# Performance work log

Measured on AMD Instinct MI355X. Metric: run time of the kernel, lower is better.

Reference implementation:

```python
import jax, jax.numpy as jnp
import numpy as np
from jax import lax

E, H, D = 1024, 16, 64          # embed_dim, num_heads, head_dim
B, T = 8, 64                    # batch, decode chunk
KV = 4096                       # kv_seq_len -> cache capacity 2*KV
START = 4096                    # start_pos (prefill already filled cache[:START])
THETA = 10000.0


def setup_inputs() -> dict:
    key = jax.random.key(0)
    kx, kck, kcv, kq, kk, kv, ko = jax.random.split(key, 7)
    s = 0.02
    return {
        "x": jax.random.normal(kx, (B, T, E), jnp.float32),
        "cache_keys": jax.random.normal(kck, (B, 2 * KV, H, D), jnp.float32),
        "cache_values": jax.random.normal(kcv, (B, 2 * KV, H, D), jnp.float32),
        "Wq": jax.random.normal(kq, (E, E), jnp.float32) * s,
        "Wk": jax.random.normal(kk, (E, E), jnp.float32) * s,
        "Wv": jax.random.normal(kv, (E, E), jnp.float32) * s,
        "Wo": jax.random.normal(ko, (E, E), jnp.float32) * s,
        "start_pos": START,
    }


def _rope_bug_faithful(x, start_pos):
    # x: (B, T, H, Dd). The source helper unpacks (B,H,T,D)=x.shape on a (B,T,H,D)
    # tensor, so rotation angles are indexed by HEAD index (positions
    # start_pos..start_pos+H-1) and broadcast over the time axis. Reproduced exactly.
    Bn, Tn, Hn, Dd = x.shape
    dh = Dd // 2
    inv_freq = 1.0 / (THETA ** (jnp.arange(dh, dtype=jnp.float32) / dh))
    pos = jnp.arange(Hn, dtype=jnp.float32) + jnp.float32(start_pos)  # (H,)
    ang = pos[:, None] * inv_freq[None, :]                            # (H, dh)
    cos = jnp.cos(ang)[None, None]                                    # (1,1,H,dh)
    sin = jnp.sin(ang)[None, None]
    xr = x.reshape(Bn, Tn, Hn, dh, 2)
    x0, x1 = xr[..., 0], xr[..., 1]
    o0 = x0 * cos - x1 * sin
    o1 = x0 * sin + x1 * cos
    return jnp.stack([o0, o1], axis=-1).reshape(Bn, Tn, Hn, Dd)


def reference(x, cache_keys, cache_values, Wq, Wk, Wv, Wo, start_pos):
    Bn, Tn, C = x.shape
    Hn, Dd = cache_keys.shape[2], cache_keys.shape[3]
    scale = 1.0 / np.sqrt(Dd).astype(np.float32)
    end = start_pos + Tn

    q = (x @ Wq).reshape(Bn, Tn, Hn, Dd)
    k = (x @ Wk).reshape(Bn, Tn, Hn, Dd)
    v = (x @ Wv).reshape(Bn, Tn, Hn, Dd)

    q = _rope_bug_faithful(q, start_pos)
    k = _rope_bug_faithful(k, start_pos)

    # cache append at dynamic offset (detached in source)
    ck = lax.dynamic_update_slice_in_dim(cache_keys, lax.stop_gradient(k), start_pos, axis=1)
    cv = lax.dynamic_update_slice_in_dim(cache_values, lax.stop_gradient(v), start_pos, axis=1)
    k_full = lax.stop_gradient(ck[:, :end])  # (B, S, H, D), S = end
    v_full = lax.stop_gradient(cv[:, :end])

    qh = q.transpose(0, 2, 1, 3)        # (B,H,T,D)
    kh = k_full.transpose(0, 2, 1, 3)   # (B,H,S,D)
    vh = v_full.transpose(0, 2, 1, 3)

    scores = jnp.einsum("bhtd,bhsd->bhts", qh, kh) * scale  # (B,H,T,S)
    i = jnp.arange(Tn)[:, None]
    j = jnp.arange(end)[None, :]
    allowed = j <= (start_pos + i)      # intended causal mask over cache span
    neg = jnp.finfo(scores.dtype).min
    scores = jnp.where(allowed[None, None], scores, neg)
    attn = jax.nn.softmax(scores, axis=-1)
    ctx = jnp.einsum("bhts,bhsd->bhtd", attn, vh)
    out = ctx.transpose(0, 2, 1, 3).reshape(Bn, Tn, C) @ Wo
    return out
```

## Files before the change

kernel.cpp:

```cpp
#include <hip/hip_runtime.h>
#include <hip/hip_bf16.h>
#include <math.h>

typedef __attribute__((ext_vector_type(8))) __bf16 bf16x8;
typedef __attribute__((ext_vector_type(4))) __bf16 bf16x4;
typedef __attribute__((ext_vector_type(4))) float f32x4;

#define EE 1024
#define HH 16
#define DD 64
#define BB 8
#define TT 64
#define NSPLIT 8

__device__ __forceinline__ f32x4 mfma16(bf16x8 a, bf16x8 b, f32x4 c) {
    return __builtin_amdgcn_mfma_f32_16x16x32_bf16(a, b, c, 0, 0, 0);
}

__global__ __launch_bounds__(256) void k_prep(const float* __restrict__ Wq, const float* __restrict__ Wk,
                                              const float* __restrict__ Wv, const float* __restrict__ Wo,
                                              __bf16* __restrict__ WT) {
    __shared__ float tile[64][68];
    int bid = blockIdx.x;
    int w = bid >> 8, tl = bid & 255;
    int k0 = (tl >> 4) * 64, n0 = (tl & 15) * 64;
    const float* W = (w == 0) ? Wq : (w == 1) ? Wk : (w == 2) ? Wv : Wo;
    int tid = threadIdx.x;
#pragma unroll
    for (int p = 0; p < 4; ++p) {
        int idx = p * 256 + tid;
        int r = idx >> 4, c4 = (idx & 15) * 4;
        float4 f = *(const float4*)&W[(size_t)(k0 + r) * EE + n0 + c4];
        *(float4*)&tile[r][c4] = f;
    }
    __syncthreads();
    __bf16* out = WT + (size_t)w * EE * EE;
#pragma unroll
    for (int p = 0; p < 2; ++p) {
        int q = p * 256 + tid;
        int r = q >> 3, c8 = (q & 7) * 8;
        bf16x8 v;
#pragma unroll
        for (int j = 0; j < 8; ++j) v[j] = (__bf16)tile[c8 + j][r];
        *(bf16x8*)&out[(size_t)(n0 + r) * EE + k0 + c8] = v;
    }
}

__global__ __launch_bounds__(256) void k_qkv(const float* __restrict__ x, const __bf16* __restrict__ WT,
                                             const int* __restrict__ sp_ptr,
                                             __bf16* __restrict__ qws, __bf16* __restrict__ knew,
                                             __bf16* __restrict__ vnew) {
    __shared__ __bf16 a_lds[64][72];
    __shared__ __bf16 b_lds[64][72];
    __shared__ float cs_l[32], sn_l[32];
    int xcd = blockIdx.x & 7, idx = blockIdx.x >> 3;
    int bn = xcd * 6 + idx % 6;
    int bm = idx / 6;
    int wsel = bn >> 4;
    int n0 = (bn & 15) * 64;
    int m0 = bm * 64;
    const __bf16* Wt = WT + (size_t)wsel * EE * EE;
    int tid = threadIdx.x;
    int wv = tid >> 6, lane = tid & 63;
    int l16 = lane & 15, lhi = lane >> 4;
    int g = tid >> 4, m4 = (tid & 15) * 4;
    int r0 = tid >> 3, c8 = (tid & 7) * 8;

    f32x4 acc[4];
#pragma unroll
    for (int f = 0; f < 4; ++f) acc[f] = (f32x4){0.f, 0.f, 0.f, 0.f};

    f32x4 areg[4];
    bf16x8 br0, br1;
#pragma unroll
    for (int p = 0; p < 4; ++p)
        areg[p] = *(const f32x4*)&x[(size_t)(m0 + p * 16 + g) * EE + m4];
    br0 = *(const bf16x8*)&Wt[(size_t)(n0 + r0) * EE + c8];
    br1 = *(const bf16x8*)&Wt[(size_t)(n0 + 32 + r0) * EE + c8];

    if (tid < 32) {
        int h = bn & 15;
        int sp = sp_ptr[0];
        float invf = powf(10000.0f, -(float)tid / 32.0f);
        float ang = (float)(sp + h) * invf;
        float s, c;
        sincosf(ang, &s, &c);
        cs_l[tid] = c;
        sn_l[tid] = s;
    }

    for (int kt = 0; kt < 16; ++kt) {
        __syncthreads();
#pragma unroll
        for (int p = 0; p < 4; ++p) {
            bf16x4 a4 = { (__bf16)areg[p][0], (__bf16)areg[p][1], (__bf16)areg[p][2], (__bf16)areg[p][3] };
            *(bf16x4*)&a_lds[p * 16 + g][m4] = a4;
        }
        *(bf16x8*)&b_lds[r0][c8] = br0;
        *(bf16x8*)&b_lds[32 + r0][c8] = br1;
        if (kt < 15) {
            int ko = (kt + 1) * 64;
#pragma unroll
            for (int p = 0; p < 4; ++p)
                areg[p] = *(const f32x4*)&x[(size_t)(m0 + p * 16 + g) * EE + ko + m4];
            br0 = *(const bf16x8*)&Wt[(size_t)(n0 + r0) * EE + ko + c8];
            br1 = *(const bf16x8*)&Wt[(size_t)(n0 + 32 + r0) * EE + ko + c8];
        }
        __syncthreads();
        bf16x8 a0 = *(bf16x8*)&a_lds[wv * 16 + l16][lhi * 8];
        bf16x8 a1 = *(bf16x8*)&a_lds[wv * 16 + l16][32 + lhi * 8];
#pragma unroll
        for (int f = 0; f < 4; ++f) {
            bf16x8 b0 = *(bf16x8*)&b_lds[f * 16 + l16][lhi * 8];
            bf16x8 b1 = *(bf16x8*)&b_lds[f * 16 + l16][32 + lhi * 8];
            acc[f] = mfma16(a0, b0, acc[f]);
            acc[f] = mfma16(a1, b1, acc[f]);
        }
    }
    __bf16* dst = (wsel == 0) ? qws : (wsel == 1) ? knew : vnew;
    int h = bn & 15;
#pragma unroll
    for (int f = 0; f < 4; ++f) {
#pragma unroll
        for (int r = 0; r < 4; ++r) {
            float v = acc[f][r];
            int row = m0 + wv * 16 + lhi * 4 + r;
            int d = f * 16 + l16;
            float o = v;
            if (wsel < 2) {
                float other = __shfl_xor(v, 1);
                int pp = d >> 1;
                float c = cs_l[pp], s = sn_l[pp];
                o = ((d & 1) == 0) ? (v * c - other * s) : (other * s + v * c);
            }
            int b = row >> 6, t = row & 63;
            dst[((size_t)((b * HH + h) * TT + t)) * DD + d] = (__bf16)o;
        }
    }
}

__global__ __launch_bounds__(256, 4) void k_attn(const __bf16* __restrict__ qws, const __bf16* __restrict__ knew,
                                                 const __bf16* __restrict__ vnew,
                                                 const float* __restrict__ ck, const float* __restrict__ cv,
                                                 __bf16* __restrict__ Opart, float* __restrict__ lpart) {
    __shared__ __bf16 k_lds[64][72];
    __shared__ __bf16 vT_lds[64][68];
    __shared__ __bf16 p_lds[64][72];
    int bh = blockIdx.x >> 3, split = blockIdx.x & 7;
    int b = bh >> 4, h = bh & 15;
    int tid = threadIdx.x, wv = tid >> 6, lane = tid & 63;
    int l16 = lane & 15, lhi = lane >> 4;
    int g = tid >> 4, m4 = (tid & 15) * 4;

    bf16x8 qf0, qf1;
    {
        const __bf16* qp = qws + ((size_t)bh * TT + (wv * 16 + l16)) * DD;
        qf0 = *(const bf16x8*)&qp[lhi * 8];
        qf1 = *(const bf16x8*)&qp[32 + lhi * 8];
    }
    f32x4 acc[4];
#pragma unroll
    for (int f = 0; f < 4; ++f) acc[f] = (f32x4){0.f, 0.f, 0.f, 0.f};
    float l[4] = {0.f, 0.f, 0.f, 0.f};

    const float* ckb = ck + (size_t)b * 8192 * EE + h * DD;
    const float* cvb = cv + (size_t)b * 8192 * EE + h * DD;
    int s0 = split * 512;

    auto compute = [&](bool mask) {
        f32x4 sf[4];
#pragma unroll
        for (int f = 0; f < 4; ++f) {
            f32x4 z = (f32x4){0.f, 0.f, 0.f, 0.f};
            bf16x8 b0 = *(bf16x8*)&k_lds[f * 16 + l16][lhi * 8];
            bf16x8 b1 = *(bf16x8*)&k_lds[f * 16 + l16][32 + lhi * 8];
            z = mfma16(qf0, b0, z);
            z = mfma16(qf1, b1, z);
            sf[f] = z;
        }
        const float SC = 0.125f * 1.44269504f;
#pragma unroll
        for (int f = 0; f < 4; ++f) {
#pragma unroll
            for (int r = 0; r < 4; ++r) {
                float sv = sf[f][r] * SC;
                if (mask) {
                    int t_row = wv * 16 + lhi * 4 + r;
                    int s_loc = f * 16 + l16;
                    if (s_loc > t_row) sv = -1e30f;
                }
                float pv = exp2f(sv);
                sf[f][r] = pv;
                l[r] += pv;
            }
        }
#pragma unroll
        for (int f = 0; f < 4; ++f)
#pragma unroll
            for (int r = 0; r < 4; ++r)
                p_lds[wv * 16 + lhi * 4 + r][f * 16 + l16] = (__bf16)sf[f][r];
        bf16x8 pa0 = *(bf16x8*)&p_lds[wv * 16 + l16][lhi * 8];
        bf16x8 pa1 = *(bf16x8*)&p_lds[wv * 16 + l16][32 + lhi * 8];
#pragma unroll
        for (int f = 0; f < 4; ++f) {
            bf16x8 v0 = *(bf16x8*)&vT_lds[f * 16 + l16][lhi * 8];
            bf16x8 v1 = *(bf16x8*)&vT_lds[f * 16 + l16][32 + lhi * 8];
            acc[f] = mfma16(pa0, v0, acc[f]);
            acc[f] = mfma16(pa1, v1, acc[f]);
        }
    };

    f32x4 kreg[4], vreg[4];
#pragma unroll
    for (int p = 0; p < 4; ++p)
        kreg[p] = *(const f32x4*)&ckb[(size_t)(s0 + p * 16 + g) * EE + m4];
#pragma unroll
    for (int i = 0; i < 4; ++i)
        vreg[i] = *(const f32x4*)&cvb[(size_t)(s0 + 4 * g + i) * EE + m4];

    for (int it = 0; it < 8; ++it) {
#pragma unroll
        for (int p = 0; p < 4; ++p) {
            bf16x4 k4 = { (__bf16)kreg[p][0], (__bf16)kreg[p][1], (__bf16)kreg[p][2], (__bf16)kreg[p][3] };
            *(bf16x4*)&k_lds[p * 16 + g][m4] = k4;
        }
#pragma unroll
        for (int j = 0; j < 4; ++j) {
            bf16x4 tv = { (__bf16)vreg[0][j], (__bf16)vreg[1][j], (__bf16)vreg[2][j], (__bf16)vreg[3][j] };
            *(bf16x4*)&vT_lds[m4 + j][4 * g] = tv;
        }
        if (it < 7) {
            int sb = s0 + (it + 1) * 64;
#pragma unroll
            for (int p = 0; p < 4; ++p)
                kreg[p] = *(const f32x4*)&ckb[(size_t)(sb + p * 16 + g) * EE + m4];
#pragma unroll
            for (int i = 0; i < 4; ++i)
                vreg[i] = *(const f32x4*)&cvb[(size_t)(sb + 4 * g + i) * EE + m4];
        }
        __syncthreads();
        compute(false);
        __syncthreads();
    }

    if (split == 7) {
#pragma unroll
        for (int p = 0; p < 2; ++p) {
            int idx = p * 256 + tid;
            int r = idx >> 3, c8 = (idx & 7) * 8;
            *(bf16x8*)&k_lds[r][c8] = *(const bf16x8*)&knew[((size_t)bh * TT + r) * DD + c8];
            bf16x8 vf = *(const bf16x8*)&vnew[((size_t)bh * TT + r) * DD + c8];
#pragma unroll
            for (int j = 0; j < 8; ++j) vT_lds[c8 + j][r] = vf[j];
        }
        __syncthreads();
        compute(true);
    }

#pragma unroll
    for (int off = 1; off < 16; off <<= 1) {
#pragma unroll
        for (int r = 0; r < 4; ++r) l[r] += __shfl_xor(l[r], off);
    }

#pragma unroll
    for (int f = 0; f < 4; ++f)
#pragma unroll
        for (int r = 0; r < 4; ++r) {
            int t = wv * 16 + lhi * 4 + r;
            int d = f * 16 + l16;
            Opart[(((size_t)split * 128 + bh) * TT + t) * DD + d] = (__bf16)acc[f][r];
        }
    if (l16 == 0) {
#pragma unroll
        for (int r = 0; r < 4; ++r) {
            int t = wv * 16 + lhi * 4 + r;
            lpart[((size_t)split * 128 + bh) * TT + t] = l[r];
        }
    }
}

__global__ __launch_bounds__(256) void k_combine(const __bf16* __restrict__ Opart, const float* __restrict__ lpart,
                                                 __bf16* __restrict__ ctxb) {
    int idx = blockIdx.x * 256 + threadIdx.x;
    int d8 = idx & 7, t = (idx >> 3) & 63, bh = idx >> 9;
    float den = 0.f, num[8];
#pragma unroll
    for (int j = 0; j < 8; ++j) num[j] = 0.f;
#pragma unroll
    for (int s = 0; s < NSPLIT; ++s) {
        den += lpart[((size_t)s * 128 + bh) * TT + t];
        bf16x8 o = *(const bf16x8*)&Opart[(((size_t)s * 128 + bh) * TT + t) * DD + d8 * 8];
#pragma unroll
        for (int j = 0; j < 8; ++j) num[j] += (float)o[j];
    }
    float inv = 1.0f / den;
    bf16x8 c;
#pragma unroll
    for (int j = 0; j < 8; ++j) c[j] = (__bf16)(num[j] * inv);
    int b = bh >> 4, h = bh & 15;
    *(bf16x8*)&ctxb[(size_t)(b * TT + t) * EE + h * DD + d8 * 8] = c;
}

__global__ __launch_bounds__(256) void k_oproj(const __bf16* __restrict__ ctxb, const __bf16* __restrict__ WoT,
                                               float* __restrict__ out) {
    __shared__ __bf16 a_lds[64][72];
    __shared__ __bf16 b_lds[64][72];
    int xcd = blockIdx.x & 7, idx = blockIdx.x >> 3;
    int bn = xcd * 2 + (idx & 1);
    int bm = idx >> 1;
    int n0 = bn * 64, m0 = bm * 64;
    int tid = threadIdx.x;
    int wv = tid >> 6, lane = tid & 63;
    int l16 = lane & 15, lhi = lane >> 4;
    int r0 = tid >> 3, c8 = (tid & 7) * 8;
    f32x4 acc[4];
#pragma unroll
    for (int f = 0; f < 4; ++f) acc[f] = (f32x4){0.f, 0.f, 0.f, 0.f};

    bf16x8 ar0 = *(const bf16x8*)&ctxb[(size_t)(m0 + r0) * EE + c8];
    bf16x8 ar1 = *(const bf16x8*)&ctxb[(size_t)(m0 + 32 + r0) * EE + c8];
    bf16x8 br0 = *(const bf16x8*)&WoT[(size_t)(n0 + r0) * EE + c8];
    bf16x8 br1 = *(const bf16x8*)&WoT[(size_t)(n0 + 32 + r0) * EE + c8];

    for (int kt = 0; kt < 16; ++kt) {
        __syncthreads();
        *(bf16x8*)&a_lds[r0][c8] = ar0;
        *(bf16x8*)&a_lds[32 + r0][c8] = ar1;
        *(bf16x8*)&b_lds[r0][c8] = br0;
        *(bf16x8*)&b_lds[32 + r0][c8] = br1;
        if (kt < 15) {
            int ko = (kt + 1) * 64;
            ar0 = *(const bf16x8*)&ctxb[(size_t)(m0 + r0) * EE + ko + c8];
            ar1 = *(const bf16x8*)&ctxb[(size_t)(m0 + 32 + r0) * EE + ko + c8];
            br0 = *(const bf16x8*)&WoT[(size_t)(n0 + r0) * EE + ko + c8];
            br1 = *(const bf16x8*)&WoT[(size_t)(n0 + 32 + r0) * EE + ko + c8];
        }
        __syncthreads();
        bf16x8 a0 = *(bf16x8*)&a_lds[wv * 16 + l16][lhi * 8];
        bf16x8 a1 = *(bf16x8*)&a_lds[wv * 16 + l16][32 + lhi * 8];
#pragma unroll
        for (int f = 0; f < 4; ++f) {
            bf16x8 b0 = *(bf16x8*)&b_lds[f * 16 + l16][lhi * 8];
            bf16x8 b1 = *(bf16x8*)&b_lds[f * 16 + l16][32 + lhi * 8];
            acc[f] = mfma16(a0, b0, acc[f]);
            acc[f] = mfma16(a1, b1, acc[f]);
        }
    }
#pragma unroll
    for (int f = 0; f < 4; ++f)
#pragma unroll
        for (int r = 0; r < 4; ++r) {
            int row = m0 + wv * 16 + lhi * 4 + r;
            out[(size_t)row * EE + n0 + f * 16 + l16] = acc[f][r];
        }
}

extern "C" void kernel_launch(void* const* d_in, const int* in_sizes, int n_in,
                              void* d_out, int out_size, void* d_ws, size_t ws_size,
                              hipStream_t stream) {
    const float* x  = (const float*)d_in[0];
    const float* ck = (const float*)d_in[1];
    const float* cv = (const float*)d_in[2];
    const float* Wq = (const float*)d_in[3];
    const float* Wk = (const float*)d_in[4];
    const float* Wv = (const float*)d_in[5];
    const float* Wo = (const float*)d_in[6];
    const int* sp   = (const int*)d_in[7];
    float* out = (float*)d_out;

    char* p = (char*)d_ws;
    __bf16* WT = (__bf16*)p;            p += (size_t)4 * 1024 * 1024 * 2;
    __bf16* qws = (__bf16*)p;           p += (size_t)524288 * 2;
    __bf16* knew = (__bf16*)p;          p += (size_t)524288 * 2;
    __bf16* vnew = (__bf16*)p;          p += (size_t)524288 * 2;
    __bf16* Opart = (__bf16*)p;         p += (size_t)NSPLIT * 128 * 64 * 64 * 2;
    float* lpart = (float*)p;           p += (size_t)NSPLIT * 8192 * 4;
    __bf16* ctxb = (__bf16*)p;          p += (size_t)524288 * 2;

    k_prep<<<1024, 256, 0, stream>>>(Wq, Wk, Wv, Wo, WT);
    k_qkv<<<384, 256, 0, stream>>>(x, WT, sp, qws, knew, vnew);
    k_attn<<<BB * HH * NSPLIT, 256, 0, stream>>>(qws, knew, vnew, ck, cv, Opart, lpart);
    k_combine<<<256, 256, 0, stream>>>(Opart, lpart, ctxb);
    k_oproj<<<128, 256, 0, stream>>>(ctxb, WT + (size_t)3 * 1024 * 1024, out);
}
```

Baseline: 84.37 us.

## Fuse Wo fp32-to-bf16 transpose into o-proj and halve its M tile

Wo is no longer pre-converted and transposed by the prep kernel. The output-projection kernel now loads fp32 Wo directly, converts it to bf16 and transposes it into shared memory. The o-proj M tile drops from 64 to 32, which doubles the grid to 256 blocks, and each wave now computes a 16x32 sub-tile. This removes a prep pass over Wo and its workspace round trip and raises o-proj parallelism. In exchange, o-proj reads fp32 Wo twice (once per M tile pair), does the conversion inline, and the attention shared-memory padding changes to 68.

```diff
diff --git a/kernel.cpp b/kernel.cpp
--- a/kernel.cpp
+++ b/kernel.cpp
@@ -18,13 +18,12 @@
 }
 
 __global__ __launch_bounds__(256) void k_prep(const float* __restrict__ Wq, const float* __restrict__ Wk,
-                                              const float* __restrict__ Wv, const float* __restrict__ Wo,
-                                              __bf16* __restrict__ WT) {
+                                              const float* __restrict__ Wv, __bf16* __restrict__ WT) {
     __shared__ float tile[64][68];
     int bid = blockIdx.x;
     int w = bid >> 8, tl = bid & 255;
     int k0 = (tl >> 4) * 64, n0 = (tl & 15) * 64;
-    const float* W = (w == 0) ? Wq : (w == 1) ? Wk : (w == 2) ? Wv : Wo;
+    const float* W = (w == 0) ? Wq : (w == 1) ? Wk : Wv;
     int tid = threadIdx.x;
 #pragma unroll
     for (int p = 0; p < 4; ++p) {
@@ -143,9 +142,9 @@
                                                  const __bf16* __restrict__ vnew,
                                                  const float* __restrict__ ck, const float* __restrict__ cv,
                                                  __bf16* __restrict__ Opart, float* __restrict__ lpart) {
-    __shared__ __bf16 k_lds[64][72];
+    __shared__ __bf16 k_lds[64][68];
     __shared__ __bf16 vT_lds[64][68];
-    __shared__ __bf16 p_lds[64][72];
+    __shared__ __bf16 p_lds[64][68];
     int bh = blockIdx.x >> 3, split = blockIdx.x & 7;
     int b = bh >> 4, h = bh & 15;
     int tid = threadIdx.x, wv = tid >> 6, lane = tid & 63;
@@ -302,57 +301,62 @@
     *(bf16x8*)&ctxb[(size_t)(b * TT + t) * EE + h * DD + d8 * 8] = c;
 }
 
-__global__ __launch_bounds__(256) void k_oproj(const __bf16* __restrict__ ctxb, const __bf16* __restrict__ WoT,
+__global__ __launch_bounds__(256) void k_oproj(const __bf16* __restrict__ ctxb, const float* __restrict__ Wo,
                                                float* __restrict__ out) {
-    __shared__ __bf16 a_lds[64][72];
-    __shared__ __bf16 b_lds[64][72];
+    __shared__ __bf16 a_lds[32][72];
+    __shared__ __bf16 b_lds[64][68];
     int xcd = blockIdx.x & 7, idx = blockIdx.x >> 3;
     int bn = xcd * 2 + (idx & 1);
     int bm = idx >> 1;
-    int n0 = bn * 64, m0 = bm * 64;
+    int n0 = bn * 64, m0 = bm * 32;
     int tid = threadIdx.x;
     int wv = tid >> 6, lane = tid & 63;
     int l16 = lane & 15, lhi = lane >> 4;
+    int g = tid >> 4, m4 = (tid & 15) * 4;
     int r0 = tid >> 3, c8 = (tid & 7) * 8;
-    f32x4 acc[4];
-#pragma unroll
-    for (int f = 0; f < 4; ++f) acc[f] = (f32x4){0.f, 0.f, 0.f, 0.f};
+    int mo = (wv & 1) * 16, no = (wv >> 1) * 32;
+    f32x4 acc[2];
+#pragma unroll
+    for (int f = 0; f < 2; ++f) acc[f] = (f32x4){0.f, 0.f, 0.f, 0.f};
 
     bf16x8 ar0 = *(const bf16x8*)&ctxb[(size_t)(m0 + r0) * EE + c8];
-    bf16x8 ar1 = *(const bf16x8*)&ctxb[(size_t)(m0 + 32 + r0) * EE + c8];
-    bf16x8 br0 = *(const bf16x8*)&WoT[(size_t)(n0 + r0) * EE + c8];
-    bf16x8 br1 = *(const bf16x8*)&WoT[(size_t)(n0 + 32 + r0) * EE + c8];
+    f32x4 breg[4];
+#pragma unroll
+    for (int i = 0; i < 4; ++i)
+        breg[i] = *(const f32x4*)&Wo[(size_t)(4 * g + i) * EE + n0 + m4];
 
     for (int kt = 0; kt < 16; ++kt) {
         __syncthreads();
         *(bf16x8*)&a_lds[r0][c8] = ar0;
-        *(bf16x8*)&a_lds[32 + r0][c8] = ar1;
-        *(bf16x8*)&b_lds[r0][c8] = br0;
-        *(bf16x8*)&b_lds[32 + r0][c8] = br1;
+#pragma unroll
+        for (int j = 0; j < 4; ++j) {
+            bf16x4 t4 = { (__bf16)breg[0][j], (__bf16)breg[1][j], (__bf16)breg[2][j], (__bf16)breg[3][j] };
+            *(bf16x4*)&b_lds[m4 + j][4 * g] = t4;
+        }
         if (kt < 15) {
             int ko = (kt + 1) * 64;
             ar0 = *(const bf16x8*)&ctxb[(size_t)(m0 + r0) * EE + ko + c8];
-            ar1 = *(const bf16x8*)&ctxb[(size_t)(m0 + 32 + r0) * EE + ko + c8];
-            br0 = *(const bf16x8*)&WoT[(size_t)(n0 + r0) * EE + ko + c8];
-            br1 = *(const bf16x8*)&WoT[(size_t)(n0 + 32 + r0) * EE + ko + c8];
-        }
-        __syncthreads();
-        bf16x8 a0 = *(bf16x8*)&a_lds[wv * 16 + l16][lhi * 8];
-        bf16x8 a1 = *(bf16x8*)&a_lds[wv * 16 + l16][32 + lhi * 8];
-#pragma unroll
-        for (int f = 0; f < 4; ++f) {
-            bf16x8 b0 = *(bf16x8*)&b_lds[f * 16 + l16][lhi * 8];
-            bf16x8 b1 = *(bf16x8*)&b_lds[f * 16 + l16][32 + lhi * 8];
+#pragma unroll
+            for (int i = 0; i < 4; ++i)
+                breg[i] = *(const f32x4*)&Wo[(size_t)(ko + 4 * g + i) * EE + n0 + m4];
+        }
+        __syncthreads();
+        bf16x8 a0 = *(bf16x8*)&a_lds[mo + l16][lhi * 8];
+        bf16x8 a1 = *(bf16x8*)&a_lds[mo + l16][32 + lhi * 8];
+#pragma unroll
+        for (int f = 0; f < 2; ++f) {
+            bf16x8 b0 = *(bf16x8*)&b_lds[no + f * 16 + l16][lhi * 8];
+            bf16x8 b1 = *(bf16x8*)&b_lds[no + f * 16 + l16][32 + lhi * 8];
             acc[f] = mfma16(a0, b0, acc[f]);
             acc[f] = mfma16(a1, b1, acc[f]);
         }
     }
 #pragma unroll
-    for (int f = 0; f < 4; ++f)
+    for (int f = 0; f < 2; ++f)
 #pragma unroll
         for (int r = 0; r < 4; ++r) {
-            int row = m0 + wv * 16 + lhi * 4 + r;
-            out[(size_t)row * EE + n0 + f * 16 + l16] = acc[f][r];
+            int row = m0 + mo + lhi * 4 + r;
+            out[(size_t)row * EE + n0 + no + f * 16 + l16] = acc[f][r];
         }
 }
 
@@ -370,7 +374,7 @@
     float* out = (float*)d_out;
 
     char* p = (char*)d_ws;
-    __bf16* WT = (__bf16*)p;            p += (size_t)4 * 1024 * 1024 * 2;
+    __bf16* WT = (__bf16*)p;            p += (size_t)3 * 1024 * 1024 * 2;
     __bf16* qws = (__bf16*)p;           p += (size_t)524288 * 2;
     __bf16* knew = (__bf16*)p;          p += (size_t)524288 * 2;
     __bf16* vnew = (__bf16*)p;          p += (size_t)524288 * 2;
@@ -378,9 +382,9 @@
     float* lpart = (float*)p;           p += (size_t)NSPLIT * 8192 * 4;
     __bf16* ctxb = (__bf16*)p;          p += (size_t)524288 * 2;
 
-    k_prep<<<1024, 256, 0, stream>>>(Wq, Wk, Wv, Wo, WT);
+    k_prep<<<768, 256, 0, stream>>>(Wq, Wk, Wv, WT);
     k_qkv<<<384, 256, 0, stream>>>(x, WT, sp, qws, knew, vnew);
     k_attn<<<BB * HH * NSPLIT, 256, 0, stream>>>(qws, knew, vnew, ck, cv, Opart, lpart);
     k_combine<<<256, 256, 0, stream>>>(Opart, lpart, ctxb);
-    k_oproj<<<128, 256, 0, stream>>>(ctxb, WT + (size_t)3 * 1024 * 1024, out);
-}
+    k_oproj<<<256, 256, 0, stream>>>(ctxb, Wo, out);
+}
```

After: 86.03 us. About the same (+2.0%).

## Fuse split-KV combine into output projection GEMM and retile to 32-wide N

Applied to the files above, without the earlier changes.

Removes the separate combine kernel and its ctx round-trip by having the output projection load the per-split partial outputs and denominators, reduce them in registers, and write the normalized A tile straight into LDS. The N tile shrinks from 64 to 32 and the grid doubles to 256 blocks for more parallelism. In exchange, each block now reads all eight split partials for its A tile, so partials are re-read once per N block (32 times instead of once). It also needs many more registers for the prefetched partials.

```diff
diff --git a/kernel.cpp b/kernel.cpp
--- a/kernel.cpp
+++ b/kernel.cpp
@@ -280,67 +280,70 @@
     }
 }
 
-__global__ __launch_bounds__(256) void k_combine(const __bf16* __restrict__ Opart, const float* __restrict__ lpart,
-                                                 __bf16* __restrict__ ctxb) {
-    int idx = blockIdx.x * 256 + threadIdx.x;
-    int d8 = idx & 7, t = (idx >> 3) & 63, bh = idx >> 9;
-    float den = 0.f, num[8];
-#pragma unroll
-    for (int j = 0; j < 8; ++j) num[j] = 0.f;
-#pragma unroll
-    for (int s = 0; s < NSPLIT; ++s) {
-        den += lpart[((size_t)s * 128 + bh) * TT + t];
-        bf16x8 o = *(const bf16x8*)&Opart[(((size_t)s * 128 + bh) * TT + t) * DD + d8 * 8];
-#pragma unroll
-        for (int j = 0; j < 8; ++j) num[j] += (float)o[j];
-    }
-    float inv = 1.0f / den;
-    bf16x8 c;
-#pragma unroll
-    for (int j = 0; j < 8; ++j) c[j] = (__bf16)(num[j] * inv);
-    int b = bh >> 4, h = bh & 15;
-    *(bf16x8*)&ctxb[(size_t)(b * TT + t) * EE + h * DD + d8 * 8] = c;
-}
-
-__global__ __launch_bounds__(256) void k_oproj(const __bf16* __restrict__ ctxb, const __bf16* __restrict__ WoT,
-                                               float* __restrict__ out) {
+__global__ __launch_bounds__(256) void k_oproj(const __bf16* __restrict__ Opart, const float* __restrict__ lpart,
+                                               const __bf16* __restrict__ WoT, float* __restrict__ out) {
     __shared__ __bf16 a_lds[64][72];
-    __shared__ __bf16 b_lds[64][72];
+    __shared__ __bf16 b_lds[32][72];
     int xcd = blockIdx.x & 7, idx = blockIdx.x >> 3;
-    int bn = xcd * 2 + (idx & 1);
-    int bm = idx >> 1;
-    int n0 = bn * 64, m0 = bm * 64;
+    int bn = xcd * 4 + (idx & 3);
+    int bq = idx >> 2;
+    int n0 = bn * 32;
     int tid = threadIdx.x;
     int wv = tid >> 6, lane = tid & 63;
     int l16 = lane & 15, lhi = lane >> 4;
     int r0 = tid >> 3, c8 = (tid & 7) * 8;
-    f32x4 acc[4];
-#pragma unroll
-    for (int f = 0; f < 4; ++f) acc[f] = (f32x4){0.f, 0.f, 0.f, 0.f};
-
-    bf16x8 ar0 = *(const bf16x8*)&ctxb[(size_t)(m0 + r0) * EE + c8];
-    bf16x8 ar1 = *(const bf16x8*)&ctxb[(size_t)(m0 + 32 + r0) * EE + c8];
-    bf16x8 br0 = *(const bf16x8*)&WoT[(size_t)(n0 + r0) * EE + c8];
-    bf16x8 br1 = *(const bf16x8*)&WoT[(size_t)(n0 + 32 + r0) * EE + c8];
+    int mo = wv * 16;
+    f32x4 acc[2];
+#pragma unroll
+    for (int f = 0; f < 2; ++f) acc[f] = (f32x4){0.f, 0.f, 0.f, 0.f};
+
+    bf16x8 oreg[2][8];
+    float dr[2][8];
+    bf16x8 brg;
+    auto loadA = [&](int head) {
+        int bh = bq * 16 + head;
+#pragma unroll
+        for (int rp = 0; rp < 2; ++rp) {
+            int t = r0 + rp * 32;
+#pragma unroll
+            for (int s = 0; s < 8; ++s) {
+                size_t base = ((size_t)(s * 128 + bh) * TT + t);
+                oreg[rp][s] = *(const bf16x8*)&Opart[base * DD + c8];
+                dr[rp][s] = lpart[base];
+            }
+        }
+    };
+    loadA(0);
+    brg = *(const bf16x8*)&WoT[(size_t)(n0 + r0) * EE + c8];
 
     for (int kt = 0; kt < 16; ++kt) {
         __syncthreads();
-        *(bf16x8*)&a_lds[r0][c8] = ar0;
-        *(bf16x8*)&a_lds[32 + r0][c8] = ar1;
-        *(bf16x8*)&b_lds[r0][c8] = br0;
-        *(bf16x8*)&b_lds[32 + r0][c8] = br1;
+#pragma unroll
+        for (int rp = 0; rp < 2; ++rp) {
+            float num[8] = {0.f, 0.f, 0.f, 0.f, 0.f, 0.f, 0.f, 0.f};
+            float den = 0.f;
+#pragma unroll
+            for (int s = 0; s < 8; ++s) {
+                den += dr[rp][s];
+#pragma unroll
+                for (int j = 0; j < 8; ++j) num[j] += (float)oreg[rp][s][j];
+            }
+            float inv = 1.0f / den;
+            bf16x8 a;
+#pragma unroll
+            for (int j = 0; j < 8; ++j) a[j] = (__bf16)(num[j] * inv);
+            *(bf16x8*)&a_lds[r0 + rp * 32][c8] = a;
+        }
+        *(bf16x8*)&b_lds[r0][c8] = brg;
         if (kt < 15) {
-            int ko = (kt + 1) * 64;
-            ar0 = *(const bf16x8*)&ctxb[(size_t)(m0 + r0) * EE + ko + c8];
-            ar1 = *(const bf16x8*)&ctxb[(size_t)(m0 + 32 + r0) * EE + ko + c8];
-            br0 = *(const bf16x8*)&WoT[(size_t)(n0 + r0) * EE + ko + c8];
-            br1 = *(const bf16x8*)&WoT[(size_t)(n0 + 32 + r0) * EE + ko + c8];
-        }
-        __syncthreads();
-        bf16x8 a0 = *(bf16x8*)&a_lds[wv * 16 + l16][lhi * 8];
-        bf16x8 a1 = *(bf16x8*)&a_lds[wv * 16 + l16][32 + lhi * 8];
-#pragma unroll
-        for (int f = 0; f < 4; ++f) {
+            loadA(kt + 1);
+            brg = *(const bf16x8*)&WoT[(size_t)(n0 + r0) * EE + (kt + 1) * 64 + c8];
+        }
+        __syncthreads();
+        bf16x8 a0 = *(bf16x8*)&a_lds[mo + l16][lhi * 8];
+        bf16x8 a1 = *(bf16x8*)&a_lds[mo + l16][32 + lhi * 8];
+#pragma unroll
+        for (int f = 0; f < 2; ++f) {
             bf16x8 b0 = *(bf16x8*)&b_lds[f * 16 + l16][lhi * 8];
             bf16x8 b1 = *(bf16x8*)&b_lds[f * 16 + l16][32 + lhi * 8];
             acc[f] = mfma16(a0, b0, acc[f]);
@@ -348,10 +351,10 @@
         }
     }
 #pragma unroll
-    for (int f = 0; f < 4; ++f)
+    for (int f = 0; f < 2; ++f)
 #pragma unroll
         for (int r = 0; r < 4; ++r) {
-            int row = m0 + wv * 16 + lhi * 4 + r;
+            int row = bq * 64 + mo + lhi * 4 + r;
             out[(size_t)row * EE + n0 + f * 16 + l16] = acc[f][r];
         }
 }
@@ -376,11 +379,9 @@
     __bf16* vnew = (__bf16*)p;          p += (size_t)524288 * 2;
     __bf16* Opart = (__bf16*)p;         p += (size_t)NSPLIT * 128 * 64 * 64 * 2;
     float* lpart = (float*)p;           p += (size_t)NSPLIT * 8192 * 4;
-    __bf16* ctxb = (__bf16*)p;          p += (size_t)524288 * 2;
 
     k_prep<<<1024, 256, 0, stream>>>(Wq, Wk, Wv, Wo, WT);
     k_qkv<<<384, 256, 0, stream>>>(x, WT, sp, qws, knew, vnew);
     k_attn<<<BB * HH * NSPLIT, 256, 0, stream>>>(qws, knew, vnew, ck, cv, Opart, lpart);
-    k_combine<<<256, 256, 0, stream>>>(Opart, lpart, ctxb);
-    k_oproj<<<128, 256, 0, stream>>>(ctxb, WT + (size_t)3 * 1024 * 1024, out);
-}
+    k_oproj<<<256, 256, 0, stream>>>(Opart, lpart, WT + (size_t)3 * 1024 * 1024, out);
+}
```

After: 97.63 us. +15.7%, slower.
